# Optimization experiments

Hardware: AMD Instinct MI355X
Metric: run time of the kernel (lower is better)

## Reference

```python
import jax, jax.numpy as jnp
import numpy as np

DT = 1.0 / 60.0  # physics timestep
NUM_BODY = 20

# ---- quaternion helpers (xyzw convention, matching the repo) ----

def quat_from_rotvec(rv):
    # rv: [..., 3] axis-angle -> quaternion [..., 4] (x,y,z,w)
    angle = jnp.linalg.norm(rv, axis=-1, keepdims=True)
    half = 0.5 * angle
    safe = jnp.where(angle < 1e-8, 1.0, angle)
    s = jnp.where(angle < 1e-8, 0.5 - angle * angle / 48.0, jnp.sin(half) / safe)
    return jnp.concatenate([rv * s, jnp.cos(half)], axis=-1)


def flip_quat_by_w(q):
    return jnp.where(q[..., 3:4] < 0, -q, q)


def quat_to_vec6d(q):
    # first two columns of the rotation matrix, row-major flattened -> [..., 6]
    x, y, z, w = q[..., 0], q[..., 1], q[..., 2], q[..., 3]
    r00 = 1 - 2 * (y * y + z * z)
    r10 = 2 * (x * y + z * w)
    r20 = 2 * (x * z - y * w)
    r01 = 2 * (x * y - z * w)
    r11 = 1 - 2 * (x * x + z * z)
    r21 = 2 * (y * z + x * w)
    return jnp.stack([r00, r01, r10, r11, r20, r21], axis=-1)


def quat_apply(q, v):
    # rotate v [..., 3] by quaternion q [..., 4]; broadcasts over leading dims
    xyz, w = q[..., :3], q[..., 3:4]
    t = 2.0 * jnp.cross(xyz, v)
    return v + w * t + jnp.cross(xyz, t)


def quat_multiply(p, q):
    pv, pw = p[..., :3], p[..., 3:4]
    qv, qw = q[..., :3], q[..., 3:4]
    v = pw * qv + qw * pv + jnp.cross(pv, qv)
    w = pw * qw - jnp.sum(pv * qv, axis=-1, keepdims=True)
    return jnp.concatenate([v, w], axis=-1)


def quat_integrate(q, omega, dt):
    # q_{t+1} = normalize(q + 0.5*dt * (omega_quat * q))
    omega_q = jnp.concatenate([omega, jnp.zeros_like(omega[..., :1])], axis=-1)
    dq = quat_multiply(omega_q, q)
    r = q + 0.5 * dt * dq
    return r / jnp.linalg.norm(r, axis=-1, keepdims=True)


def integrate_state(state, delta, dt):
    # state: [B, NB, 13] = pos(3) | rot quat(4) | vel(3) | avel(3)
    B, NB, _ = state.shape
    pos, rot = state[..., 0:3], state[..., 3:7]
    vel, avel = state[..., 7:10], state[..., 10:13]
    root_rot = state[:, 0:1, 3:7]                       # [B, 1, 4]
    d3 = delta.reshape(B, -1, 3)                        # [B, 2*NB, 3]
    true_d = quat_apply(root_rot, d3).reshape(B, NB, 6)
    lin, ang = true_d[..., :3], true_d[..., 3:]
    next_vel = vel + lin
    next_avel = avel + ang
    next_pos = pos + next_vel * dt
    next_rot = quat_integrate(rot, next_avel, dt)
    return jnp.concatenate([next_pos, next_rot, next_vel, next_avel], axis=-1)


def setup_inputs() -> dict:
    key = jax.random.key(0)
    ks = jax.random.split(key, 12)
    B = 32768
    inp = {
        "state": jax.random.normal(ks[0], (B, NUM_BODY, 13), jnp.float32),
        "action": jax.random.normal(ks[1], (B, 57), jnp.float32),
        "n_observation": jax.random.normal(ks[2], (B, 300), jnp.float32),
        "W1": jax.random.normal(ks[3], (414, 512), jnp.float32) * 0.05,
        "b1": jax.random.normal(ks[4], (512,), jnp.float32) * 0.05,
        "W2": jax.random.normal(ks[5], (512, 512), jnp.float32) * 0.05,
        "b2": jax.random.normal(ks[6], (512,), jnp.float32) * 0.05,
        "W3": jax.random.normal(ks[7], (512, 120), jnp.float32) * 0.05,
        "b3": jax.random.normal(ks[8], (120,), jnp.float32) * 0.05,
        "delta_mean": jax.random.normal(ks[9], (120,), jnp.float32) * 0.01,
        "delta_std": jax.random.uniform(ks[10], (120,), jnp.float32) + 0.5,
    }
    return inp


def reference(state, action, n_observation, W1, b1, W2, b2, W3, b3, delta_mean, delta_std):
    B = action.shape[0]
    # action rotvecs -> quats -> 6d representation
    aq = flip_quat_by_w(quat_from_rotvec(action.reshape(-1, 3)))
    a6 = quat_to_vec6d(aq).reshape(B, -1)               # [B, 114]
    x = jnp.concatenate([n_observation, a6], axis=-1)   # [B, 414]
    h = jax.nn.relu(x @ W1 + b1)
    h = jax.nn.relu(h @ W2 + b2)
    n_delta = h @ W3 + b3                                # [B, 120]
    delta = n_delta * delta_std + delta_mean             # unnormalize
    return integrate_state(state, delta, DT)
```

## Files before the change

### kernel.cpp

```cpp
#include <hip/hip_runtime.h>
#include <hip/hip_bf16.h>
#include <math.h>

#define DT (1.0f / 60.0f)

typedef __bf16 bf16x8 __attribute__((ext_vector_type(8)));
typedef float f32x4 __attribute__((ext_vector_type(4)));

#define XSTRIDE 848
#define HSTRIDE 1040
#define DLSTRIDE 124

struct __attribute__((packed)) f4u {
    float x, y, z, w;
};

__global__ __launch_bounds__(256) void prep_weights(
    const float* __restrict__ W1, const float* __restrict__ W2,
    const float* __restrict__ W3, __hip_bfloat16* __restrict__ W1p,
    __hip_bfloat16* __restrict__ W2p, __hip_bfloat16* __restrict__ W3p) {
    int idx = blockIdx.x * 256 + threadIdx.x;
    if (idx < 212992) {
        int d = idx;
        int e = d & 7, l = (d >> 3) & 63, t = d >> 9;
        int nt = t & 31, ks = t >> 5;
        int n = nt * 16 + (l & 15);
        int k = ks * 32 + (l >> 4) * 8 + e;
        W1p[d] = __float2bfloat16(k < 414 ? W1[k * 512 + n] : 0.0f);
        return;
    }
    idx -= 212992;
    if (idx < 262144) {
        int d = idx;
        int e = d & 7, l = (d >> 3) & 63, t = d >> 9;
        int nt = t & 31, ks = t >> 5;
        int n = nt * 16 + (l & 15);
        int k = ks * 32 + (l >> 4) * 8 + e;
        W2p[d] = __float2bfloat16(W2[k * 512 + n]);
        return;
    }
    idx -= 262144;
    if (idx < 65536) {
        int d = idx;
        int e = d & 7, l = (d >> 3) & 63, t = d >> 9;
        int nt = t & 7, ks = t >> 3;
        int n = nt * 16 + (l & 15);
        int k = ks * 32 + (l >> 4) * 8 + e;
        W3p[d] = __float2bfloat16(n < 120 ? W3[k * 120 + n] : 0.0f);
    }
}

template <int KSTEPS, int NT, int JF, int ASTRIDE, bool FRAG>
__device__ __forceinline__ void mlp_layer(const char* Abase, const char* Bbase,
                                          int laneOff, f32x4 (&acc)[4][JF],
                                          bf16x8 (&wpre)[JF]) {
    bf16x8 w[JF];
#pragma unroll
    for (int j = 0; j < JF; j++) w[j] = wpre[j];
#pragma unroll 2
    for (int ks = 0; ks < KSTEPS; ks++) {
        bf16x8 ax[4];
#pragma unroll
        for (int i = 0; i < 4; i++) {
            if (FRAG)
                ax[i] = *(const bf16x8*)(Abase + (((ks << 2) + i) << 10));
            else
                ax[i] = *(const bf16x8*)(Abase + ks * 64 + i * 16 * ASTRIDE);
        }
#pragma unroll
        for (int i = 0; i < 4; i++)
#pragma unroll
            for (int j = 0; j < JF; j++)
                acc[i][j] = __builtin_amdgcn_mfma_f32_16x16x32_bf16(
                    w[j], ax[i], acc[i][j], 0, 0, 0);
        if (ks + 1 < KSTEPS) {
#pragma unroll
            for (int j = 0; j < JF; j++)
                w[j] = *(const bf16x8*)(Bbase + (((ks + 1) * NT + j) << 10) + laneOff);
        }
    }
}

__device__ __forceinline__ void store_h_relu_fr(const f32x4 (&acc)[4][4],
                                                char* smem, const float* bias,
                                                int wn, int lrow, int kgrp) {
#pragma unroll
    for (int j = 0; j < 4; j++) {
        int f = wn * 64 + j * 16 + kgrp * 4;
        float4 bb = *(const float4*)(bias + f);
        int fragbase = (f >> 5) << 2;
        int off = lrow * 16 + (((f >> 3) & 3) << 8) + ((f & 7) << 1);
#pragma unroll
        for (int i = 0; i < 4; i++) {
            float v0 = acc[i][j][0] + bb.x;
            float v1 = acc[i][j][1] + bb.y;
            float v2 = acc[i][j][2] + bb.z;
            float v3 = acc[i][j][3] + bb.w;
            v0 = v0 > 0.0f ? v0 : 0.0f;
            v1 = v1 > 0.0f ? v1 : 0.0f;
            v2 = v2 > 0.0f ? v2 : 0.0f;
            v3 = v3 > 0.0f ? v3 : 0.0f;
            union { __hip_bfloat162 h2[2]; uint2 u; } pk;
            pk.h2[0] = __float22bfloat162_rn(make_float2(v0, v1));
            pk.h2[1] = __float22bfloat162_rn(make_float2(v2, v3));
            *(uint2*)(smem + ((fragbase + i) << 10) + off) = pk.u;
        }
    }
}

__device__ __forceinline__ void quat_apply3(float qx, float qy, float qz,
                                            float qw, float vx, float vy,
                                            float vz, float& ox, float& oy,
                                            float& oz) {
    float tx = 2.0f * (qy * vz - qz * vy);
    float ty = 2.0f * (qz * vx - qx * vz);
    float tz = 2.0f * (qx * vy - qy * vx);
    ox = vx + qw * tx + (qy * tz - qz * ty);
    oy = vy + qw * ty + (qz * tx - qx * tz);
    oz = vz + qw * tz + (qx * ty - qy * tx);
}

__global__ __launch_bounds__(512, 4) void fused_mlp(
    const float* __restrict__ obs, const float* __restrict__ action,
    const __hip_bfloat16* __restrict__ W1p, const float* __restrict__ b1,
    const __hip_bfloat16* __restrict__ W2p, const float* __restrict__ b2,
    const __hip_bfloat16* __restrict__ W3p, const float* __restrict__ b3,
    const float* __restrict__ dstd, const float* __restrict__ dmean,
    const float* __restrict__ state, float* __restrict__ out) {
    alignas(16) __shared__ char smem[64 * HSTRIDE];
    const int tid = threadIdx.x;
    const int blk = blockIdx.x;
    const int lane = tid & 63, wn = tid >> 6;
    const int lrow = lane & 15, kgrp = lane >> 4;
    const int laneOff = lane * 16;

    bf16x8 wpre[4];
#pragma unroll
    for (int j = 0; j < 4; j++)
        wpre[j] = *(const bf16x8*)((const char*)W1p + (wn << 12) + (j << 10) + laneOff);

    {
        const float4* og = (const float4*)obs + (size_t)blk * 64 * 75;
#pragma unroll
        for (int i = 0; i < 10; i++) {
            int f = tid + i * 512;
            if (f < 4800) {
                int row = f / 75;
                int c4 = f - row * 75;
                float4 v = og[f];
                union { __hip_bfloat162 h2[2]; uint2 u; } pk;
                pk.h2[0] = __float22bfloat162_rn(make_float2(v.x, v.y));
                pk.h2[1] = __float22bfloat162_rn(make_float2(v.z, v.w));
                *(uint2*)(smem + row * XSTRIDE + c4 * 8) = pk.u;
            }
        }
#pragma unroll
        for (int i = 0; i < 3; i++) {
            int q = tid + i * 512;
            if (q < 1216) {
                int row = q / 19;
                int j = q - row * 19;
                const float* a = action + ((size_t)(blk * 64 + row)) * 57 + j * 3;
                float rx = a[0], ry = a[1], rz = a[2];
                float ang = sqrtf(rx * rx + ry * ry + rz * rz);
                float half = 0.5f * ang;
                float s;
                if (ang < 1e-8f)
                    s = 0.5f - ang * ang * (1.0f / 48.0f);
                else
                    s = __sinf(half) / ang;
                float qx = rx * s, qy = ry * s, qz = rz * s, qw = __cosf(half);
                union { __hip_bfloat16 h[6]; uint u[3]; } pq;
                pq.h[0] = __float2bfloat16(1.0f - 2.0f * (qy * qy + qz * qz));
                pq.h[1] = __float2bfloat16(2.0f * (qx * qy - qz * qw));
                pq.h[2] = __float2bfloat16(2.0f * (qx * qy + qz * qw));
                pq.h[3] = __float2bfloat16(1.0f - 2.0f * (qx * qx + qz * qz));
                pq.h[4] = __float2bfloat16(2.0f * (qx * qz - qy * qw));
                pq.h[5] = __float2bfloat16(2.0f * (qy * qz + qx * qw));
                char* p = smem + row * XSTRIDE + 600 + j * 12;
                *(uint*)p = pq.u[0];
                *(uint*)(p + 4) = pq.u[1];
                *(uint*)(p + 8) = pq.u[2];
            }
        }
        if (tid < 320) {
            int row = tid / 5;
            int p = tid - row * 5;
            *(uint*)(smem + row * XSTRIDE + 828 + p * 4) = 0u;
        }
    }
    __syncthreads();

    f32x4 acc[4][4];
    f32x4 zero4 = {0.0f, 0.0f, 0.0f, 0.0f};
#pragma unroll
    for (int i = 0; i < 4; i++)
#pragma unroll
        for (int j = 0; j < 4; j++) acc[i][j] = zero4;

    mlp_layer<13, 32, 4, XSTRIDE, false>(smem + lrow * XSTRIDE + kgrp * 16,
                                         (const char*)W1p + (wn << 12),
                                         laneOff, acc, wpre);
#pragma unroll
    for (int j = 0; j < 4; j++)
        wpre[j] = *(const bf16x8*)((const char*)W2p + (wn << 12) + (j << 10) + laneOff);
    __syncthreads();
    store_h_relu_fr(acc, smem, b1, wn, lrow, kgrp);
    __syncthreads();

#pragma unroll
    for (int i = 0; i < 4; i++)
#pragma unroll
        for (int j = 0; j < 4; j++) acc[i][j] = zero4;
    mlp_layer<16, 32, 4, 0, true>(smem + laneOff,
                                  (const char*)W2p + (wn << 12), laneOff, acc,
                                  wpre);
    const char* Bb3 = (const char*)W3p + (wn << 10);
    bf16x8 c0 = *(const bf16x8*)(Bb3 + laneOff);
    __syncthreads();
    store_h_relu_fr(acc, smem, b2, wn, lrow, kgrp);
    __syncthreads();

    f4u ps0[3], ps1[3], ps2[3], prq[3];
    float ps12[3];
#pragma unroll
    for (int it = 0; it < 3; it++) {
        int idx = tid + it * 512;
        if (idx < 1280) {
            int lr = idx / 20;
            int body = idx - lr * 20;
            const float* sb = state + ((size_t)(blk * 64 + lr)) * 260 + body * 13;
            const float* rq = state + ((size_t)(blk * 64 + lr)) * 260 + 3;
            ps0[it] = *(const f4u*)sb;
            ps1[it] = *(const f4u*)(sb + 4);
            ps2[it] = *(const f4u*)(sb + 8);
            ps12[it] = sb[12];
            prq[it] = *(const f4u*)rq;
        }
    }

    f32x4 a3[4];
#pragma unroll
    for (int i = 0; i < 4; i++) a3[i] = zero4;
    {
        const char* Afr = smem + laneOff;
        bf16x8 c1;
#pragma unroll 2
        for (int ks = 0; ks < 16; ks++) {
            if (ks + 1 < 16) {
                if ((ks & 1) == 0)
                    c1 = *(const bf16x8*)(Bb3 + ((ks + 1) << 13) + laneOff);
                else
                    c0 = *(const bf16x8*)(Bb3 + ((ks + 1) << 13) + laneOff);
            }
            bf16x8 ax[4];
#pragma unroll
            for (int i = 0; i < 4; i++)
                ax[i] = *(const bf16x8*)(Afr + (((ks << 2) + i) << 10));
#pragma unroll
            for (int i = 0; i < 4; i++)
                a3[i] = __builtin_amdgcn_mfma_f32_16x16x32_bf16(
                    (ks & 1) ? c1 : c0, ax[i], a3[i], 0, 0, 0);
        }
    }
    __syncthreads();

    float* dl = (float*)smem;
    {
        int f = wn * 16 + kgrp * 4;
        if (f < 120) {
            float4 bb = *(const float4*)(b3 + f);
            float4 sc = *(const float4*)(dstd + f);
            float4 mn = *(const float4*)(dmean + f);
#pragma unroll
            for (int i = 0; i < 4; i++) {
                int row = i * 16 + lrow;
                float4 dv;
                dv.x = (a3[i][0] + bb.x) * sc.x + mn.x;
                dv.y = (a3[i][1] + bb.y) * sc.y + mn.y;
                dv.z = (a3[i][2] + bb.z) * sc.z + mn.z;
                dv.w = (a3[i][3] + bb.w) * sc.w + mn.w;
                *(float4*)(dl + row * DLSTRIDE + f) = dv;
            }
        }
    }
    __syncthreads();

    float ov[3][13];
#pragma unroll
    for (int it = 0; it < 3; it++) {
        int idx = tid + it * 512;
        if (idx < 1280) {
            int lr = idx / 20;
            int body = idx - lr * 20;
            float qx = prq[it].x, qy = prq[it].y, qz = prq[it].z, qw = prq[it].w;
            const float* d = dl + lr * DLSTRIDE + body * 6;

            float lx, ly, lz, ax, ay, az;
            quat_apply3(qx, qy, qz, qw, d[0], d[1], d[2], lx, ly, lz);
            quat_apply3(qx, qy, qz, qw, d[3], d[4], d[5], ax, ay, az);

            float vx = ps1[it].w + lx, vy = ps2[it].x + ly, vz = ps2[it].y + lz;
            float wx = ps2[it].z + ax, wy = ps2[it].w + ay, wz = ps12[it] + az;
            float px = ps0[it].x + vx * DT, py = ps0[it].y + vy * DT,
                  pz = ps0[it].z + vz * DT;

            float rx = ps0[it].w, ry = ps1[it].x, rz = ps1[it].y, rw = ps1[it].z;
            float dqx = rw * wx + (wy * rz - wz * ry);
            float dqy = rw * wy + (wz * rx - wx * rz);
            float dqz = rw * wz + (wx * ry - wy * rx);
            float dqw = -(wx * rx + wy * ry + wz * rz);
            float h = 0.5f * DT;
            float nx = rx + h * dqx, ny = ry + h * dqy, nz = rz + h * dqz,
                  nw = rw + h * dqw;
            float inv = 1.0f / sqrtf(nx * nx + ny * ny + nz * nz + nw * nw);

            ov[it][0] = px;
            ov[it][1] = py;
            ov[it][2] = pz;
            ov[it][3] = nx * inv;
            ov[it][4] = ny * inv;
            ov[it][5] = nz * inv;
            ov[it][6] = nw * inv;
            ov[it][7] = vx;
            ov[it][8] = vy;
            ov[it][9] = vz;
            ov[it][10] = wx;
            ov[it][11] = wy;
            ov[it][12] = wz;
        }
    }
    __syncthreads();

#pragma unroll
    for (int it = 0; it < 3; it++) {
        int idx = tid + it * 512;
        if (idx < 1280) {
            int lr = idx / 20;
            int body = idx - lr * 20;
            float* dst = (float*)(smem + lr * 1040 + body * 52);
#pragma unroll
            for (int k = 0; k < 13; k++) dst[k] = ov[it][k];
        }
    }
    __syncthreads();

    {
        float4* og = (float4*)(out + (size_t)blk * 64 * 260);
#pragma unroll
        for (int i = 0; i < 9; i++) {
            int f = tid + i * 512;
            if (f < 4160) {
                og[f] = *(const float4*)(smem + f * 16);
            }
        }
    }
}

extern "C" void kernel_launch(void* const* d_in, const int* in_sizes, int n_in,
                              void* d_out, int out_size, void* d_ws,
                              size_t ws_size, hipStream_t stream) {
    const float* state = (const float*)d_in[0];
    const float* action = (const float*)d_in[1];
    const float* obs = (const float*)d_in[2];
    const float* W1 = (const float*)d_in[3];
    const float* b1 = (const float*)d_in[4];
    const float* W2 = (const float*)d_in[5];
    const float* b2 = (const float*)d_in[6];
    const float* W3 = (const float*)d_in[7];
    const float* b3 = (const float*)d_in[8];
    const float* dmean = (const float*)d_in[9];
    const float* dstd = (const float*)d_in[10];
    float* out = (float*)d_out;
    char* ws = (char*)d_ws;

    const int B = in_sizes[1] / 57;

    __hip_bfloat16* W1p = (__hip_bfloat16*)(ws);
    __hip_bfloat16* W2p = (__hip_bfloat16*)(ws + 425984);
    __hip_bfloat16* W3p = (__hip_bfloat16*)(ws + 950272);

    prep_weights<<<2112, 256, 0, stream>>>(W1, W2, W3, W1p, W2p, W3p);
    fused_mlp<<<B / 64, 512, 0, stream>>>(obs, action, W1p, b1, W2p, b2, W3p,
                                          b3, dstd, dmean, state, out);
}
```

Before: 163.3 us.

## Shrink row tile to 32 rows with 4 waves each covering 128 columns

Each block now handles 32 batch rows with 256 threads instead of 64 rows with 512 threads. Each wave computes 2 row-tiles by 8 column-tiles rather than 4 by 4. The goal is to double the block count and halve shared memory so more blocks fit per CU and the grid covers the GPU better. In exchange, each weight fragment is reused across fewer rows, so total weight traffic per batch row doubles, and the wider accumulator raises register pressure.

```diff
diff --git a/kernel.cpp b/kernel.cpp
--- a/kernel.cpp
+++ b/kernel.cpp
@@ -8,8 +8,9 @@
 typedef float f32x4 __attribute__((ext_vector_type(4)));
 
 #define XSTRIDE 848
-#define HSTRIDE 1040
 #define DLSTRIDE 124
+#define ROWS 32
+#define SMEMB 33280
 
 struct __attribute__((packed)) f4u {
     float x, y, z, w;
@@ -50,25 +51,25 @@
     }
 }
 
-template <int KSTEPS, int NT, int JF, int ASTRIDE, bool FRAG>
+template <int KSTEPS, int NT, int JF, int RT, int ASTRIDE, bool FRAG>
 __device__ __forceinline__ void mlp_layer(const char* Abase, const char* Bbase,
-                                          int laneOff, f32x4 (&acc)[4][JF],
+                                          int laneOff, f32x4 (&acc)[RT][JF],
                                           bf16x8 (&wpre)[JF]) {
     bf16x8 w[JF];
 #pragma unroll
     for (int j = 0; j < JF; j++) w[j] = wpre[j];
 #pragma unroll 2
     for (int ks = 0; ks < KSTEPS; ks++) {
-        bf16x8 ax[4];
-#pragma unroll
-        for (int i = 0; i < 4; i++) {
+        bf16x8 ax[RT];
+#pragma unroll
+        for (int i = 0; i < RT; i++) {
             if (FRAG)
-                ax[i] = *(const bf16x8*)(Abase + (((ks << 2) + i) << 10));
+                ax[i] = *(const bf16x8*)(Abase + ((ks * RT + i) << 10));
             else
                 ax[i] = *(const bf16x8*)(Abase + ks * 64 + i * 16 * ASTRIDE);
         }
 #pragma unroll
-        for (int i = 0; i < 4; i++)
+        for (int i = 0; i < RT; i++)
 #pragma unroll
             for (int j = 0; j < JF; j++)
                 acc[i][j] = __builtin_amdgcn_mfma_f32_16x16x32_bf16(
@@ -81,17 +82,17 @@
     }
 }
 
-__device__ __forceinline__ void store_h_relu_fr(const f32x4 (&acc)[4][4],
+__device__ __forceinline__ void store_h_relu_fr(const f32x4 (&acc)[2][8],
                                                 char* smem, const float* bias,
                                                 int wn, int lrow, int kgrp) {
 #pragma unroll
-    for (int j = 0; j < 4; j++) {
-        int f = wn * 64 + j * 16 + kgrp * 4;
+    for (int j = 0; j < 8; j++) {
+        int f = wn * 128 + j * 16 + kgrp * 4;
         float4 bb = *(const float4*)(bias + f);
-        int fragbase = (f >> 5) << 2;
+        int fragbase = (f >> 5) << 1;
         int off = lrow * 16 + (((f >> 3) & 3) << 8) + ((f & 7) << 1);
 #pragma unroll
-        for (int i = 0; i < 4; i++) {
+        for (int i = 0; i < 2; i++) {
             float v0 = acc[i][j][0] + bb.x;
             float v1 = acc[i][j][1] + bb.y;
             float v2 = acc[i][j][2] + bb.z;
@@ -120,31 +121,31 @@
     oz = vz + qw * tz + (qx * ty - qy * tx);
 }
 
-__global__ __launch_bounds__(512, 4) void fused_mlp(
+__global__ __launch_bounds__(256, 4) void fused_mlp(
     const float* __restrict__ obs, const float* __restrict__ action,
     const __hip_bfloat16* __restrict__ W1p, const float* __restrict__ b1,
     const __hip_bfloat16* __restrict__ W2p, const float* __restrict__ b2,
     const __hip_bfloat16* __restrict__ W3p, const float* __restrict__ b3,
     const float* __restrict__ dstd, const float* __restrict__ dmean,
     const float* __restrict__ state, float* __restrict__ out) {
-    alignas(16) __shared__ char smem[64 * HSTRIDE];
+    alignas(16) __shared__ char smem[SMEMB];
     const int tid = threadIdx.x;
     const int blk = blockIdx.x;
     const int lane = tid & 63, wn = tid >> 6;
     const int lrow = lane & 15, kgrp = lane >> 4;
     const int laneOff = lane * 16;
 
-    bf16x8 wpre[4];
-#pragma unroll
-    for (int j = 0; j < 4; j++)
-        wpre[j] = *(const bf16x8*)((const char*)W1p + (wn << 12) + (j << 10) + laneOff);
+    bf16x8 wpre[8];
+#pragma unroll
+    for (int j = 0; j < 8; j++)
+        wpre[j] = *(const bf16x8*)((const char*)W1p + (wn << 13) + (j << 10) + laneOff);
 
     {
-        const float4* og = (const float4*)obs + (size_t)blk * 64 * 75;
+        const float4* og = (const float4*)obs + (size_t)blk * ROWS * 75;
 #pragma unroll
         for (int i = 0; i < 10; i++) {
-            int f = tid + i * 512;
-            if (f < 4800) {
+            int f = tid + i * 256;
+            if (f < ROWS * 75) {
                 int row = f / 75;
                 int c4 = f - row * 75;
                 float4 v = og[f];
@@ -156,11 +157,11 @@
         }
 #pragma unroll
         for (int i = 0; i < 3; i++) {
-            int q = tid + i * 512;
-            if (q < 1216) {
+            int q = tid + i * 256;
+            if (q < ROWS * 19) {
                 int row = q / 19;
                 int j = q - row * 19;
-                const float* a = action + ((size_t)(blk * 64 + row)) * 57 + j * 3;
+                const float* a = action + ((size_t)(blk * ROWS + row)) * 57 + j * 3;
                 float rx = a[0], ry = a[1], rz = a[2];
                 float ang = sqrtf(rx * rx + ry * ry + rz * rz);
                 float half = 0.5f * ang;
@@ -183,7 +184,7 @@
                 *(uint*)(p + 8) = pq.u[2];
             }
         }
-        if (tid < 320) {
+        if (tid < ROWS * 5) {
             int row = tid / 5;
             int p = tid - row * 5;
             *(uint*)(smem + row * XSTRIDE + 828 + p * 4) = 0u;
@@ -191,32 +192,35 @@
     }
     __syncthreads();
 
-    f32x4 acc[4][4];
+    f32x4 acc[2][8];
     f32x4 zero4 = {0.0f, 0.0f, 0.0f, 0.0f};
 #pragma unroll
-    for (int i = 0; i < 4; i++)
-#pragma unroll
-        for (int j = 0; j < 4; j++) acc[i][j] = zero4;
-
-    mlp_layer<13, 32, 4, XSTRIDE, false>(smem + lrow * XSTRIDE + kgrp * 16,
-                                         (const char*)W1p + (wn << 12),
-                                         laneOff, acc, wpre);
-#pragma unroll
-    for (int j = 0; j < 4; j++)
-        wpre[j] = *(const bf16x8*)((const char*)W2p + (wn << 12) + (j << 10) + laneOff);
+    for (int i = 0; i < 2; i++)
+#pragma unroll
+        for (int j = 0; j < 8; j++) acc[i][j] = zero4;
+
+    mlp_layer<13, 32, 8, 2, XSTRIDE, false>(smem + lrow * XSTRIDE + kgrp * 16,
+                                            (const char*)W1p + (wn << 13),
+                                            laneOff, acc, wpre);
+#pragma unroll
+    for (int j = 0; j < 8; j++)
+        wpre[j] = *(const bf16x8*)((const char*)W2p + (wn << 13) + (j << 10) + laneOff);
     __syncthreads();
     store_h_relu_fr(acc, smem, b1, wn, lrow, kgrp);
     __syncthreads();
 
 #pragma unroll
-    for (int i = 0; i < 4; i++)
-#pragma unroll
-        for (int j = 0; j < 4; j++) acc[i][j] = zero4;
-    mlp_layer<16, 32, 4, 0, true>(smem + laneOff,
-                                  (const char*)W2p + (wn << 12), laneOff, acc,
-                                  wpre);
-    const char* Bb3 = (const char*)W3p + (wn << 10);
-    bf16x8 c0 = *(const bf16x8*)(Bb3 + laneOff);
+    for (int i = 0; i < 2; i++)
+#pragma unroll
+        for (int j = 0; j < 8; j++) acc[i][j] = zero4;
+    mlp_layer<16, 32, 8, 2, 0, true>(smem + laneOff,
+                                     (const char*)W2p + (wn << 13), laneOff,
+                                     acc, wpre);
+    const char* Bb3 = (const char*)W3p;
+    bf16x8 c[2];
+#pragma unroll
+    for (int j = 0; j < 2; j++)
+        c[j] = *(const bf16x8*)(Bb3 + ((wn * 2 + j) << 10) + laneOff);
     __syncthreads();
     store_h_relu_fr(acc, smem, b2, wn, lrow, kgrp);
     __syncthreads();
@@ -225,12 +229,12 @@
     float ps12[3];
 #pragma unroll
     for (int it = 0; it < 3; it++) {
-        int idx = tid + it * 512;
-        if (idx < 1280) {
+        int idx = tid + it * 256;
+        if (idx < ROWS * 20) {
             int lr = idx / 20;
             int body = idx - lr * 20;
-            const float* sb = state + ((size_t)(blk * 64 + lr)) * 260 + body * 13;
-            const float* rq = state + ((size_t)(blk * 64 + lr)) * 260 + 3;
+            const float* sb = state + ((size_t)(blk * ROWS + lr)) * 260 + body * 13;
+            const float* rq = state + ((size_t)(blk * ROWS + lr)) * 260 + 3;
             ps0[it] = *(const f4u*)sb;
             ps1[it] = *(const f4u*)(sb + 4);
             ps2[it] = *(const f4u*)(sb + 8);
@@ -239,47 +243,50 @@
         }
     }
 
-    f32x4 a3[4];
-#pragma unroll
-    for (int i = 0; i < 4; i++) a3[i] = zero4;
+    f32x4 a3[2][2];
+#pragma unroll
+    for (int i = 0; i < 2; i++)
+#pragma unroll
+        for (int j = 0; j < 2; j++) a3[i][j] = zero4;
     {
         const char* Afr = smem + laneOff;
-        bf16x8 c1;
 #pragma unroll 2
         for (int ks = 0; ks < 16; ks++) {
+            bf16x8 ax[2];
+#pragma unroll
+            for (int i = 0; i < 2; i++)
+                ax[i] = *(const bf16x8*)(Afr + ((ks * 2 + i) << 10));
+#pragma unroll
+            for (int i = 0; i < 2; i++)
+#pragma unroll
+                for (int j = 0; j < 2; j++)
+                    a3[i][j] = __builtin_amdgcn_mfma_f32_16x16x32_bf16(
+                        c[j], ax[i], a3[i][j], 0, 0, 0);
             if (ks + 1 < 16) {
-                if ((ks & 1) == 0)
-                    c1 = *(const bf16x8*)(Bb3 + ((ks + 1) << 13) + laneOff);
-                else
-                    c0 = *(const bf16x8*)(Bb3 + ((ks + 1) << 13) + laneOff);
-            }
-            bf16x8 ax[4];
-#pragma unroll
-            for (int i = 0; i < 4; i++)
-                ax[i] = *(const bf16x8*)(Afr + (((ks << 2) + i) << 10));
-#pragma unroll
-            for (int i = 0; i < 4; i++)
-                a3[i] = __builtin_amdgcn_mfma_f32_16x16x32_bf16(
-                    (ks & 1) ? c1 : c0, ax[i], a3[i], 0, 0, 0);
+#pragma unroll
+                for (int j = 0; j < 2; j++)
+                    c[j] = *(const bf16x8*)(Bb3 + (((ks + 1) * 8 + wn * 2 + j) << 10) + laneOff);
+            }
         }
     }
     __syncthreads();
 
     float* dl = (float*)smem;
-    {
-        int f = wn * 16 + kgrp * 4;
+#pragma unroll
+    for (int j = 0; j < 2; j++) {
+        int f = wn * 32 + j * 16 + kgrp * 4;
         if (f < 120) {
             float4 bb = *(const float4*)(b3 + f);
             float4 sc = *(const float4*)(dstd + f);
             float4 mn = *(const float4*)(dmean + f);
 #pragma unroll
-            for (int i = 0; i < 4; i++) {
+            for (int i = 0; i < 2; i++) {
                 int row = i * 16 + lrow;
                 float4 dv;
-                dv.x = (a3[i][0] + bb.x) * sc.x + mn.x;
-                dv.y = (a3[i][1] + bb.y) * sc.y + mn.y;
-                dv.z = (a3[i][2] + bb.z) * sc.z + mn.z;
-                dv.w = (a3[i][3] + bb.w) * sc.w + mn.w;
+                dv.x = (a3[i][j][0] + bb.x) * sc.x + mn.x;
+                dv.y = (a3[i][j][1] + bb.y) * sc.y + mn.y;
+                dv.z = (a3[i][j][2] + bb.z) * sc.z + mn.z;
+                dv.w = (a3[i][j][3] + bb.w) * sc.w + mn.w;
                 *(float4*)(dl + row * DLSTRIDE + f) = dv;
             }
         }
@@ -289,8 +296,8 @@
     float ov[3][13];
 #pragma unroll
     for (int it = 0; it < 3; it++) {
-        int idx = tid + it * 512;
-        if (idx < 1280) {
+        int idx = tid + it * 256;
+        if (idx < ROWS * 20) {
             int lr = idx / 20;
             int body = idx - lr * 20;
             float qx = prq[it].x, qy = prq[it].y, qz = prq[it].z, qw = prq[it].w;
@@ -334,8 +341,8 @@
 
 #pragma unroll
     for (int it = 0; it < 3; it++) {
-        int idx = tid + it * 512;
-        if (idx < 1280) {
+        int idx = tid + it * 256;
+        if (idx < ROWS * 20) {
             int lr = idx / 20;
             int body = idx - lr * 20;
             float* dst = (float*)(smem + lr * 1040 + body * 52);
@@ -346,11 +353,11 @@
     __syncthreads();
 
     {
-        float4* og = (float4*)(out + (size_t)blk * 64 * 260);
+        float4* og = (float4*)(out + (size_t)blk * ROWS * 260);
 #pragma unroll
         for (int i = 0; i < 9; i++) {
-            int f = tid + i * 512;
-            if (f < 4160) {
+            int f = tid + i * 256;
+            if (f < ROWS * 65) {
                 og[f] = *(const float4*)(smem + f * 16);
             }
         }
@@ -381,6 +388,6 @@
     __hip_bfloat16* W3p = (__hip_bfloat16*)(ws + 950272);
 
     prep_weights<<<2112, 256, 0, stream>>>(W1, W2, W3, W1p, W2p, W3p);
-    fused_mlp<<<B / 64, 512, 0, stream>>>(obs, action, W1p, b1, W2p, b2, W3p,
-                                          b3, dstd, dmean, state, out);
-}
+    fused_mlp<<<B / ROWS, 256, 0, stream>>>(obs, action, W1p, b1, W2p, b2,
+                                            W3p, b3, dstd, dmean, state, out);
+}
```

New measurement: 187.1 us. 14.6% more time.
